# Kernel tuning notes

Hardware: AMD Instinct MI355X
Metric: run time of the kernel (lower is better)

The kernel has to match this reference:

```python
import jax, jax.numpy as jnp
import numpy as np

N_NODES = 512
HEADS = 4
CO = 64        # per-head out channels (PyG GATConv out_channels)
NEG_SLOPE = 0.2  # PyG GATConv default negative_slope


def setup_inputs() -> dict:
    key = jax.random.key(0)
    k0, k1, k2, k3, k4 = jax.random.split(key, 5)
    B, C, T, N = 8, 64, 12, N_NODES
    E = 8192
    x = jax.random.normal(k0, (B, C, T, N), dtype=jnp.float32)
    edge_index = jax.random.randint(k1, (2, E), 0, N, dtype=jnp.int32)
    # learned params of GATConv(in=64, out=64, heads=4, concat=False)
    W = jax.random.normal(k2, (C, HEADS * CO), dtype=jnp.float32) / np.sqrt(C).astype(np.float32)
    att_src = jax.random.normal(k3, (HEADS, CO), dtype=jnp.float32) * 0.1
    att_dst = jax.random.normal(k4, (HEADS, CO), dtype=jnp.float32) * 0.1
    bias = jnp.zeros((CO,), dtype=jnp.float32)
    return {"x": x, "edge_index": edge_index, "W": W,
            "att_src": att_src, "att_dst": att_dst, "bias": bias}


def reference(x, edge_index, W, att_src, att_dst, bias):
    # x: [B, C, T, N] -> batch of G = B*T graphs, all sharing edge_index.
    B, C, T, N = x.shape
    H, Co = att_src.shape
    G = B * T
    xg = x.transpose(0, 2, 3, 1).reshape(G, N, C)              # [G,N,C]
    h = (xg @ W).reshape(G, N, H, Co)                          # [G,N,H,Co]
    a_src = jnp.einsum('gnhc,hc->gnh', h, att_src)             # [G,N,H]
    a_dst = jnp.einsum('gnhc,hc->gnh', h, att_dst)             # [G,N,H]
    # add self loops (PyG GATConv default)
    loops = jnp.arange(N, dtype=edge_index.dtype)
    src = jnp.concatenate([edge_index[0], loops])              # [E']
    dst = jnp.concatenate([edge_index[1], loops])              # [E']
    # attention logits per edge, leading edge axis for segment ops
    logits = jax.nn.leaky_relu(a_src[:, src] + a_dst[:, dst], NEG_SLOPE)  # [G,E',H]
    logits = logits.transpose(1, 0, 2)                         # [E',G,H]
    m = jax.ops.segment_max(logits, dst, num_segments=N)       # [N,G,H]
    e = jnp.exp(logits - m[dst])
    s = jax.ops.segment_sum(e, dst, num_segments=N)            # [N,G,H]
    alpha = e / s[dst]                                         # [E',G,H]  (dropout off: eval)
    msg = alpha[..., None] * h[:, src].transpose(1, 0, 2, 3)   # [E',G,H,Co]
    out = jax.ops.segment_sum(msg, dst, num_segments=N)        # [N,G,H,Co]
    out = out.mean(axis=2) + bias                              # [N,G,Co]  concat=False -> head mean
    out = out.transpose(1, 0, 2).reshape(B, T, N, Co)          # [B,T,N,Co]
    return out.transpose(0, 3, 1, 2)                           # [B,Co,T,N]
```

## Files before the change

### kernel.cpp

```cpp
#include <hip/hip_runtime.h>

#define B_  8
#define C_  64
#define T_  12
#define N_  512
#define E_  8192
#define H_  4
#define CO_ 64
#define G_  (B_ * T_)
#define EP_ (E_ + N_)
#define MAXDEG 128
#define MDW    48
#define POISON 0xAAAAAAAAu

typedef __bf16 bf16x8 __attribute__((ext_vector_type(8)));
typedef unsigned short usx8 __attribute__((ext_vector_type(8)));
typedef float  f32x4  __attribute__((ext_vector_type(4)));

static __device__ __forceinline__ unsigned short f2bf(float f) {
    unsigned int u = __float_as_uint(f);
    return (unsigned short)((u + 0x7fffu + ((u >> 16) & 1u)) >> 16);
}
static __device__ __forceinline__ float lo16f(unsigned int u) {
    return (float)__builtin_bit_cast(_Float16, (unsigned short)(u & 0xffffu));
}
static __device__ __forceinline__ float hi16f(unsigned int u) {
    return (float)__builtin_bit_cast(_Float16, (unsigned short)(u >> 16));
}

__global__ __launch_bounds__(256) void k_prep(
    const float* __restrict__ x, const int* __restrict__ ei,
    const float* __restrict__ W,
    const float* __restrict__ att_src, const float* __restrict__ att_dst,
    unsigned short* __restrict__ xtb, float* __restrict__ as_, float* __restrict__ ad_,
    unsigned int* __restrict__ cnt, int* __restrict__ srclist,
    unsigned short* __restrict__ Wfrag)
{
    int bid = blockIdx.x, tid = threadIdx.x;

    if (bid >= 768) {
        if (bid < 800) {
            int e = (bid - 768) * 256 + tid;
            int d = ei[E_ + e], s = ei[e];
            unsigned int pos = atomicAdd(&cnt[d], 1u) - POISON;
            srclist[d * MAXDEG + pos] = s;
        } else {
            int base = (bid - 800) * 2048;
            #pragma unroll
            for (int it = 0; it < 8; ++it) {
                int idx = base + it * 256 + tid;
                int c  = idx >> 8, r = idx & 255;
                int hh = r >> 6,  co = r & 63;
                int k  = hh * 64 + c;
                int ks = k >> 5, kq = (k >> 3) & 3, j = k & 7;
                int nt = co >> 4, l = kq * 16 + (co & 15);
                Wfrag[(size_t)((ks * 4 + nt) * 64 + l) * 8 + j] = f2bf(W[idx]);
            }
        }
        return;
    }

    __shared__ float xs[64][65];
    __shared__ float Wls[64][4], Wld[64][4];
    __shared__ float sa[64][5], sd[64][5];

    int lane = tid & 63, q = tid >> 6;

    {
        const float4* W4 = reinterpret_cast<const float4*>(W);
        const float4* A4 = reinterpret_cast<const float4*>(att_src);
        const float4* D4 = reinterpret_cast<const float4*>(att_dst);
        float4 uu = A4[lane];
        float4 vv = D4[lane];
        #pragma unroll
        for (int it = 0; it < 16; ++it) {
            int idx4 = tid + it * 256;
            float4 w = W4[idx4];
            float s1 = w.x*uu.x + w.y*uu.y + w.z*uu.z + w.w*uu.w;
            float s2 = w.x*vv.x + w.y*vv.y + w.z*vv.z + w.w*vv.w;
            #pragma unroll
            for (int off = 1; off < 16; off <<= 1) {
                s1 += __shfl_xor(s1, off, 64);
                s2 += __shfl_xor(s2, off, 64);
            }
            if ((lane & 15) == 0) {
                Wls[q + it * 4][lane >> 4] = s1;
                Wld[q + it * 4][lane >> 4] = s2;
            }
        }
    }

    int g  = bid >> 3, tl = bid & 7;
    int b  = g / T_, t = g - b * T_;
    int n0 = tl * 64;

    #pragma unroll
    for (int i = 0; i < 16; ++i) {
        int c = q + i * 4;
        xs[c][lane] = x[((size_t)(b * C_ + c) * T_ + t) * N_ + n0 + lane];
    }
    __syncthreads();

    float s1 = 0.f, s2 = 0.f;
    for (int c = 0; c < 64; ++c) {
        float v = xs[c][lane];
        s1 += v * Wls[c][q];
        s2 += v * Wld[c][q];
    }
    sa[lane][q] = s1;
    sd[lane][q] = s2;

    #pragma unroll
    for (int i = 0; i < 16; ++i) {
        int nl = q + i * 4;
        xtb[((size_t)(g * N_ + n0 + nl)) * 64 + lane] = f2bf(xs[lane][nl]);
    }
    __syncthreads();

    int nl = tid >> 2, hh = tid & 3;
    as_[((size_t)(g * N_ + n0 + nl)) * 4 + hh] = sa[nl][hh];
    ad_[((size_t)(g * N_ + n0 + nl)) * 4 + hh] = sd[nl][hh];
}

__global__ __launch_bounds__(256, 3) void k_fused(
    const unsigned short* __restrict__ xtb, const float* __restrict__ as_,
    const float* __restrict__ ad_,
    const unsigned int* __restrict__ cnt, const int* __restrict__ srclist,
    const unsigned short* __restrict__ Wfrag, const float* __restrict__ bias,
    float* __restrict__ out)
{
    __shared__ __align__(16) char lds[36864];
    unsigned int*   wbu = reinterpret_cast<unsigned int*>(lds + 32768);
    unsigned short* ssu = reinterpret_cast<unsigned short*>(lds + 35840);
    float (*tl)[65] = reinterpret_cast<float (*)[65]>(lds);

    int bid  = blockIdx.x;
    int xcd  = bid & 7, rest = bid >> 3;
    int gq   = rest % 12, tile = rest / 12;
    int g    = xcd * 12 + gq;
    int n0   = tile * 64;
    int b    = g / T_, t = g - b * T_;
    int tid  = threadIdx.x;
    int wave = tid >> 6, lane = tid & 63;
    int fslot = tid >> 5;
    int t32  = tid & 31;
    int hp   = t32 & 1;
    int fp   = t32 >> 1;
    int hl   = lane & 31;
    int ch2  = hl * 2;

    const unsigned short* xg = xtb + ((size_t)g * N_) * 64 + ch2;
    const float2* as2 = reinterpret_cast<const float2*>(as_) + (size_t)g * N_ * 2;
    const float2* ad2 = reinterpret_cast<const float2*>(ad_) + (size_t)g * N_ * 2;

    struct Stage {
        int dt, dtfr, scnt, node;
        int se[3];
        float2 sav[3];
        float2 adv;
    };

    auto do_stage = [&](int q, Stage& S) {
        int node = n0 + (fslot >> 1) * 16 + q * 2 + (fslot & 1);
        int dg = (int)(cnt[node] - POISON);
        dg = min(dg, MDW - 2);
        S.dt = dg + 1;
        int pm = max(S.dt, __shfl_xor(S.dt, 32, 64));
        pm = __builtin_amdgcn_readfirstlane(pm);
        S.dtfr = (pm + 7) & ~7;
        S.node = node;
        S.adv  = ad2[(size_t)node * 2 + hp];
        S.scnt = 0;
        #pragma unroll
        for (int i = 0; i < 3; ++i) {
            int e = fp + i * 16;
            if (e < S.dt) {
                int s = (e < dg) ? srclist[node * MAXDEG + e] : node;
                S.se[i]  = s;
                S.sav[i] = as2[(size_t)s * 2 + hp];
                S.scnt = i + 1;
            }
        }
    };

    auto do_fill = [&](const Stage& S) {
        #pragma unroll
        for (int i = 0; i < 3; ++i) {
            if (i < S.scnt) {
                int e = fp + i * 16;
                float v0 = S.sav[i].x + S.adv.x; v0 = v0 > 0.f ? v0 : 0.2f * v0;
                float v1 = S.sav[i].y + S.adv.y; v1 = v1 > 0.f ? v1 : 0.2f * v1;
                auto ph = __builtin_amdgcn_cvt_pkrtz(__expf(v0), __expf(v1));
                wbu[(fslot * MDW + e) * 2 + hp] = __builtin_bit_cast(unsigned int, ph);
                if (hp == 0) ssu[fslot * MDW + e] = (unsigned short)S.se[i];
            }
        }
        for (int e = S.dt + t32; e < S.dtfr; e += 32) {
            wbu[(fslot * MDW + e) * 2 + 0] = 0u;
            wbu[(fslot * MDW + e) * 2 + 1] = 0u;
            ssu[fslot * MDW + e] = (unsigned short)S.node;
        }
    };

    Stage cur, nxt;
    do_stage(0, cur);
    do_fill(cur);

    for (int p = 0; p < 8; ++p) {
        if (p < 7) do_stage(p + 1, nxt);

        const unsigned short* srow = ssu + fslot * MDW;
        const uint2* wrow = reinterpret_cast<const uint2*>(wbu + fslot * MDW * 2);
        int dtfr = cur.dtfr;

        float zA0=0.f, zA1=0.f, zA2=0.f, zA3=0.f;
        float zB0=0.f, zB1=0.f, zB2=0.f, zB3=0.f;
        float s0=0.f, s1=0.f, s2=0.f, s3=0.f;

        uint4 ssv = *reinterpret_cast<const uint4*>(srow);
        unsigned int xv[8];
        {
            unsigned int sw4[4] = {ssv.x, ssv.y, ssv.z, ssv.w};
            #pragma unroll
            for (int j = 0; j < 8; ++j) {
                unsigned int si = (j & 1) ? (sw4[j >> 1] >> 16) : (sw4[j >> 1] & 0xffffu);
                xv[j] = *reinterpret_cast<const unsigned int*>(xg + (size_t)si * 64);
            }
        }
        for (int e = 8; e <= dtfr; e += 8) {
            unsigned int xv2[8];
            if (e < dtfr) {
                uint4 ssv2 = *reinterpret_cast<const uint4*>(srow + e);
                unsigned int sw4[4] = {ssv2.x, ssv2.y, ssv2.z, ssv2.w};
                #pragma unroll
                for (int j = 0; j < 8; ++j) {
                    unsigned int si = (j & 1) ? (sw4[j >> 1] >> 16) : (sw4[j >> 1] & 0xffffu);
                    xv2[j] = *reinterpret_cast<const unsigned int*>(xg + (size_t)si * 64);
                }
            }
            const uint2* wp = wrow + (e - 8);
            #pragma unroll
            for (int j = 0; j < 8; ++j) {
                uint2 wq = wp[j];
                float wa = lo16f(wq.x), wb_ = hi16f(wq.x);
                float wc = lo16f(wq.y), wd  = hi16f(wq.y);
                float x0 = __uint_as_float(xv[j] << 16);
                float x1 = __uint_as_float(xv[j] & 0xffff0000u);
                zA0 += wa * x0;  zB0 += wa * x1;  s0 += wa;
                zA1 += wb_ * x0; zB1 += wb_ * x1; s1 += wb_;
                zA2 += wc * x0;  zB2 += wc * x1;  s2 += wc;
                zA3 += wd * x0;  zB3 += wd * x1;  s3 += wd;
            }
            if (e < dtfr) {
                #pragma unroll
                for (int j = 0; j < 8; ++j) xv[j] = xv2[j];
            }
        }

        int nl = cur.node - n0;

        if (p < 7) { do_fill(nxt); }

        float r0 = __builtin_amdgcn_rcpf(s0), r1 = __builtin_amdgcn_rcpf(s1);
        float r2 = __builtin_amdgcn_rcpf(s2), r3 = __builtin_amdgcn_rcpf(s3);
        unsigned int sw = (unsigned int)((nl & 7) << 4);
        unsigned int o0 = (unsigned int)(nl * 512 + ch2 * 2);
        unsigned int p0 = (unsigned int)f2bf(zA0 * r0) | ((unsigned int)f2bf(zB0 * r0) << 16);
        unsigned int p1 = (unsigned int)f2bf(zA1 * r1) | ((unsigned int)f2bf(zB1 * r1) << 16);
        unsigned int p2 = (unsigned int)f2bf(zA2 * r2) | ((unsigned int)f2bf(zB2 * r2) << 16);
        unsigned int p3 = (unsigned int)f2bf(zA3 * r3) | ((unsigned int)f2bf(zB3 * r3) << 16);
        *reinterpret_cast<unsigned int*>(lds + ((o0 +   0) ^ sw)) = p0;
        *reinterpret_cast<unsigned int*>(lds + ((o0 + 128) ^ sw)) = p1;
        *reinterpret_cast<unsigned int*>(lds + ((o0 + 256) ^ sw)) = p2;
        *reinterpret_cast<unsigned int*>(lds + ((o0 + 384) ^ sw)) = p3;

        if (p < 7) cur = nxt;
    }

    int m = lane & 15, quad = lane >> 4;
    int nrow = wave * 16 + m;
    unsigned int swr = (unsigned int)((m & 7) << 4);

    f32x4 acc[4];
    #pragma unroll
    for (int nt = 0; nt < 4; ++nt) acc[nt] = (f32x4){0.f, 0.f, 0.f, 0.f};

    #pragma unroll
    for (int ks = 0; ks < 8; ++ks) {
        unsigned int ro = (unsigned int)(nrow * 512 + quad * 16 + ks * 64);
        uint4 za = *reinterpret_cast<const uint4*>(lds + (ro ^ swr));
        bf16x8 a = __builtin_bit_cast(bf16x8, za);
        #pragma unroll
        for (int nt = 0; nt < 4; ++nt) {
            usx8 ub = *reinterpret_cast<const usx8*>(
                Wfrag + (size_t)(((ks * 4 + nt) * 64 + lane) * 8));
            bf16x8 bw = __builtin_bit_cast(bf16x8, ub);
            acc[nt] = __builtin_amdgcn_mfma_f32_16x16x32_bf16(a, bw, acc[nt], 0, 0, 0);
        }
    }
    __syncthreads();

    #pragma unroll
    for (int nt = 0; nt < 4; ++nt) {
        int co = nt * 16 + m;
        float bv = bias[co];
        #pragma unroll
        for (int rr = 0; rr < 4; ++rr) {
            int row = wave * 16 + quad * 4 + rr;
            tl[row][co] = 0.25f * acc[nt][rr] + bv;
        }
    }
    __syncthreads();

    #pragma unroll
    for (int it = 0; it < 16; ++it) {
        int c = wave + it * 4;
        out[((size_t)(b * CO_ + c) * T_ + t) * N_ + n0 + lane] = tl[lane][c];
    }
}

extern "C" void kernel_launch(void* const* d_in, const int* in_sizes, int n_in,
                              void* d_out, int out_size, void* d_ws, size_t ws_size,
                              hipStream_t stream) {
    const float* x       = (const float*)d_in[0];
    const int*   ei      = (const int*)  d_in[1];
    const float* W       = (const float*)d_in[2];
    const float* att_src = (const float*)d_in[3];
    const float* att_dst = (const float*)d_in[4];
    const float* bias    = (const float*)d_in[5];
    float* out = (float*)d_out;

    char* p = (char*)d_ws;
    unsigned short* xtb = (unsigned short*)p; p += (size_t)G_ * N_ * C_ * sizeof(unsigned short);
    float* as_     = (float*)p;  p += (size_t)G_ * N_ * H_ * sizeof(float);
    float* ad_     = (float*)p;  p += (size_t)G_ * N_ * H_ * sizeof(float);
    unsigned short* Wfrag = (unsigned short*)p; p += 64 * 256 * sizeof(unsigned short);
    unsigned int* cnt = (unsigned int*)p; p += 512 * sizeof(unsigned int);
    int* srclist   = (int*)p;    p += N_ * MAXDEG * sizeof(int);

    k_prep  <<<808, 256, 0, stream>>>(x, ei, W, att_src, att_dst,
                                      xtb, as_, ad_, cnt, srclist, Wfrag);
    k_fused <<<768, 256, 0, stream>>>(xtb, as_, ad_, cnt, srclist, Wfrag, bias, out);
}
```

Baseline: 117.1 us.

## Shrink node tiles in prep and fused kernels to raise grid parallelism

The prep kernel now handles 32 nodes per block instead of 64, doubling its grid, and splits the attention dot products across 8 thread groups. The fused kernel handles 16 destination nodes per block instead of 64, with two pipelined stages instead of eight. Each wave now does one MFMA output tile, LDS use drops, and occupancy is raised to 6 blocks per SM. The aim is to fill the GPU better and cut per-block serial latency. The cost is more blocks, repeated per-block W preprocessing in prep, and less prefetch overlap.

```diff
diff --git a/kernel.cpp b/kernel.cpp
--- a/kernel.cpp
+++ b/kernel.cpp
@@ -38,14 +38,14 @@
 {
     int bid = blockIdx.x, tid = threadIdx.x;
 
-    if (bid >= 768) {
-        if (bid < 800) {
-            int e = (bid - 768) * 256 + tid;
+    if (bid >= 1536) {
+        if (bid < 1568) {
+            int e = (bid - 1536) * 256 + tid;
             int d = ei[E_ + e], s = ei[e];
             unsigned int pos = atomicAdd(&cnt[d], 1u) - POISON;
             srclist[d * MAXDEG + pos] = s;
         } else {
-            int base = (bid - 800) * 2048;
+            int base = (bid - 1568) * 2048;
             #pragma unroll
             for (int it = 0; it < 8; ++it) {
                 int idx = base + it * 256 + tid;
@@ -60,9 +60,9 @@
         return;
     }
 
-    __shared__ float xs[64][65];
+    __shared__ float xs[64][33];
     __shared__ float Wls[64][4], Wld[64][4];
-    __shared__ float sa[64][5], sd[64][5];
+    __shared__ float sa[32][9];
 
     int lane = tid & 63, q = tid >> 6;
 
@@ -90,55 +90,57 @@
         }
     }
 
-    int g  = bid >> 3, tl = bid & 7;
+    int g  = bid >> 4, tl = bid & 15;
     int b  = g / T_, t = g - b * T_;
-    int n0 = tl * 64;
+    int n0 = tl * 32;
+
+    int n = tid & 31, cq = tid >> 5;
 
     #pragma unroll
-    for (int i = 0; i < 16; ++i) {
-        int c = q + i * 4;
-        xs[c][lane] = x[((size_t)(b * C_ + c) * T_ + t) * N_ + n0 + lane];
-    }
-    __syncthreads();
-
-    float s1 = 0.f, s2 = 0.f;
-    for (int c = 0; c < 64; ++c) {
-        float v = xs[c][lane];
-        s1 += v * Wls[c][q];
-        s2 += v * Wld[c][q];
-    }
-    sa[lane][q] = s1;
-    sd[lane][q] = s2;
+    for (int i = 0; i < 8; ++i) {
+        int c = cq * 8 + i;
+        xs[c][n] = x[((size_t)(b * C_ + c) * T_ + t) * N_ + n0 + n];
+    }
+    __syncthreads();
+
+    {
+        const float (*Wp)[4] = (cq >> 2) ? Wld : Wls;
+        int h = cq & 3;
+        float s = 0.f;
+        for (int c = 0; c < 64; ++c) s += xs[c][n] * Wp[c][h];
+        sa[n][cq] = s;
+    }
 
     #pragma unroll
-    for (int i = 0; i < 16; ++i) {
-        int nl = q + i * 4;
-        xtb[((size_t)(g * N_ + n0 + nl)) * 64 + lane] = f2bf(xs[lane][nl]);
-    }
-    __syncthreads();
-
-    int nl = tid >> 2, hh = tid & 3;
-    as_[((size_t)(g * N_ + n0 + nl)) * 4 + hh] = sa[nl][hh];
-    ad_[((size_t)(g * N_ + n0 + nl)) * 4 + hh] = sd[nl][hh];
-}
-
-__global__ __launch_bounds__(256, 3) void k_fused(
+    for (int i = 0; i < 8; ++i) {
+        int n2 = q * 8 + i;
+        xtb[((size_t)(g * N_ + n0 + n2)) * 64 + lane] = f2bf(xs[lane][n2]);
+    }
+    __syncthreads();
+
+    int n3 = tid >> 3, k = tid & 7;
+    float v = sa[n3][k];
+    float* dst = (k >> 2) ? ad_ : as_;
+    dst[((size_t)(g * N_ + n0 + n3)) * 4 + (k & 3)] = v;
+}
+
+__global__ __launch_bounds__(256, 6) void k_fused(
     const unsigned short* __restrict__ xtb, const float* __restrict__ as_,
     const float* __restrict__ ad_,
     const unsigned int* __restrict__ cnt, const int* __restrict__ srclist,
     const unsigned short* __restrict__ Wfrag, const float* __restrict__ bias,
     float* __restrict__ out)
 {
-    __shared__ __align__(16) char lds[36864];
-    unsigned int*   wbu = reinterpret_cast<unsigned int*>(lds + 32768);
-    unsigned short* ssu = reinterpret_cast<unsigned short*>(lds + 35840);
+    __shared__ __align__(16) char lds[12032];
+    unsigned int*   wbu = reinterpret_cast<unsigned int*>(lds + 8192);
+    unsigned short* ssu = reinterpret_cast<unsigned short*>(lds + 11264);
     float (*tl)[65] = reinterpret_cast<float (*)[65]>(lds);
 
     int bid  = blockIdx.x;
     int xcd  = bid & 7, rest = bid >> 3;
     int gq   = rest % 12, tile = rest / 12;
     int g    = xcd * 12 + gq;
-    int n0   = tile * 64;
+    int n0   = tile * 16;
     int b    = g / T_, t = g - b * T_;
     int tid  = threadIdx.x;
     int wave = tid >> 6, lane = tid & 63;
@@ -160,8 +162,8 @@
         float2 adv;
     };
 
-    auto do_stage = [&](int q, Stage& S) {
-        int node = n0 + (fslot >> 1) * 16 + q * 2 + (fslot & 1);
+    auto do_stage = [&](int qq, Stage& S) {
+        int node = n0 + fslot * 2 + qq;
         int dg = (int)(cnt[node] - POISON);
         dg = min(dg, MDW - 2);
         S.dt = dg + 1;
@@ -206,8 +208,8 @@
     do_stage(0, cur);
     do_fill(cur);
 
-    for (int p = 0; p < 8; ++p) {
-        if (p < 7) do_stage(p + 1, nxt);
+    for (int p = 0; p < 2; ++p) {
+        if (p < 1) do_stage(1, nxt);
 
         const unsigned short* srow = ssu + fslot * MDW;
         const uint2* wrow = reinterpret_cast<const uint2*>(wbu + fslot * MDW * 2);
@@ -259,7 +261,7 @@
 
         int nl = cur.node - n0;
 
-        if (p < 7) { do_fill(nxt); }
+        if (p < 1) { do_fill(nxt); }
 
         float r0 = __builtin_amdgcn_rcpf(s0), r1 = __builtin_amdgcn_rcpf(s1);
         float r2 = __builtin_amdgcn_rcpf(s2), r3 = __builtin_amdgcn_rcpf(s3);
@@ -274,48 +276,46 @@
         *reinterpret_cast<unsigned int*>(lds + ((o0 + 256) ^ sw)) = p2;
         *reinterpret_cast<unsigned int*>(lds + ((o0 + 384) ^ sw)) = p3;
 
-        if (p < 7) cur = nxt;
-    }
+        if (p < 1) cur = nxt;
+    }
+
+    __syncthreads();
 
     int m = lane & 15, quad = lane >> 4;
-    int nrow = wave * 16 + m;
     unsigned int swr = (unsigned int)((m & 7) << 4);
-
-    f32x4 acc[4];
-    #pragma unroll
-    for (int nt = 0; nt < 4; ++nt) acc[nt] = (f32x4){0.f, 0.f, 0.f, 0.f};
-
+    int nt = wave;
+
+    f32x4 acc = (f32x4){0.f, 0.f, 0.f, 0.f};
     #pragma unroll
     for (int ks = 0; ks < 8; ++ks) {
-        unsigned int ro = (unsigned int)(nrow * 512 + quad * 16 + ks * 64);
+        unsigned int ro = (unsigned int)(m * 512 + quad * 16 + ks * 64);
         uint4 za = *reinterpret_cast<const uint4*>(lds + (ro ^ swr));
         bf16x8 a = __builtin_bit_cast(bf16x8, za);
-        #pragma unroll
-        for (int nt = 0; nt < 4; ++nt) {
-            usx8 ub = *reinterpret_cast<const usx8*>(
-                Wfrag + (size_t)(((ks * 4 + nt) * 64 + lane) * 8));
-            bf16x8 bw = __builtin_bit_cast(bf16x8, ub);
-            acc[nt] = __builtin_amdgcn_mfma_f32_16x16x32_bf16(a, bw, acc[nt], 0, 0, 0);
-        }
-    }
-    __syncthreads();
-
-    #pragma unroll
-    for (int nt = 0; nt < 4; ++nt) {
+        usx8 ub = *reinterpret_cast<const usx8*>(
+            Wfrag + (size_t)(((ks * 4 + nt) * 64 + lane) * 8));
+        bf16x8 bw = __builtin_bit_cast(bf16x8, ub);
+        acc = __builtin_amdgcn_mfma_f32_16x16x32_bf16(a, bw, acc, 0, 0, 0);
+    }
+    __syncthreads();
+
+    {
         int co = nt * 16 + m;
         float bv = bias[co];
         #pragma unroll
         for (int rr = 0; rr < 4; ++rr) {
-            int row = wave * 16 + quad * 4 + rr;
-            tl[row][co] = 0.25f * acc[nt][rr] + bv;
-        }
-    }
-    __syncthreads();
-
-    #pragma unroll
-    for (int it = 0; it < 16; ++it) {
-        int c = wave + it * 4;
-        out[((size_t)(b * CO_ + c) * T_ + t) * N_ + n0 + lane] = tl[lane][c];
+            int row = quad * 4 + rr;
+            tl[row][co] = 0.25f * acc[rr] + bv;
+        }
+    }
+    __syncthreads();
+
+    {
+        int nl2 = tid & 15, cb = tid >> 4;
+        #pragma unroll
+        for (int it = 0; it < 4; ++it) {
+            int c = cb + it * 16;
+            out[((size_t)(b * CO_ + c) * T_ + t) * N_ + n0 + nl2] = tl[nl2][c];
+        }
     }
 }
 
@@ -338,7 +338,7 @@
     unsigned int* cnt = (unsigned int*)p; p += 512 * sizeof(unsigned int);
     int* srclist   = (int*)p;    p += N_ * MAXDEG * sizeof(int);
 
-    k_prep  <<<808, 256, 0, stream>>>(x, ei, W, att_src, att_dst,
-                                      xtb, as_, ad_, cnt, srclist, Wfrag);
-    k_fused <<<768, 256, 0, stream>>>(xtb, as_, ad_, cnt, srclist, Wfrag, bias, out);
-}
+    k_prep  <<<1576, 256, 0, stream>>>(x, ei, W, att_src, att_dst,
+                                       xtb, as_, ad_, cnt, srclist, Wfrag);
+    k_fused <<<3072, 256, 0, stream>>>(xtb, as_, ad_, cnt, srclist, Wfrag, bias, out);
+}
```

Measured after the change: 132.9 us. 1.14x slower.
